# Optimization experiments

Hardware: AMD Instinct MI355X
Metric: run time of the kernel (lower is better)

## Reference

```python
import jax, jax.numpy as jnp
import numpy as np

# ---- problem dims (match init_kwargs / input_specs) ----
MC = 2048        # max_concepts
D = 128          # embed_dim
B = 64           # batch
L = 16           # program length
NOBJ = 128       # objects per scene
FDIM = 512       # feature_dim
NN = MC + NOBJ   # num_nodes
TEMP = 3.0       # cosine temperature
TH = 0.8         # true_th (cosine, train==val)
POS = 10.0
NEG = -10.0
YES_IDX = 0      # protocol['concepts','yes']
NO_IDX = 1       # protocol['concepts','no']
INIT_VAR = 0.001


def setup_inputs() -> dict:
    key = jax.random.key(0)
    ks = jax.random.split(key, 6)
    scene = jax.random.normal(ks[0], (B, NOBJ, FDIM), jnp.float32)
    # program[:, :, 0] = op code in [0,7), program[:, :, 1] = argument index
    program = jax.random.randint(ks[1], (B, L, 2), 0, 7, dtype=jnp.int32)
    concept_table = jax.random.normal(ks[2], (MC, D), jnp.float32) * INIT_VAR
    relation_table = jax.random.normal(ks[3], (MC, D * D), jnp.float32) * INIT_VAR
    W_feat = jax.random.normal(ks[4], (FDIM, D), jnp.float32) * INIT_VAR
    b_feat = jax.random.normal(ks[5], (D,), jnp.float32) * INIT_VAR
    return {"scene": scene, "program": program, "concept_table": concept_table,
            "relation_table": relation_table, "W_feat": W_feat, "b_feat": b_feat}


def _cos_sim(x, y, eps=1e-8):
    # torch F.cosine_similarity semantics: clamp each norm at eps
    xn = jnp.maximum(jnp.linalg.norm(x, axis=-1), eps)
    yn = jnp.maximum(jnp.linalg.norm(y, axis=-1), eps)
    return jnp.sum(x * y, axis=-1) / (xn * yn)


def reference(scene, program, concept_table, relation_table, W_feat, b_feat):
    # feature_mlp (dim_hidden == 0 -> single Linear)
    objects = scene @ W_feat + b_feat                              # [B, NOBJ, D]
    # per-step embedded arguments
    concept_args = concept_table[program[:, :, 1]]                 # [B, L, D]
    rel_args = relation_table[program[:, :, 1]].reshape(B, L, D, D)
    node_is_concept = jnp.arange(NN) < MC                          # [NN]
    # all_nodes = concat(all_concepts, objects) per sample
    all_nodes = jnp.concatenate(
        [jnp.broadcast_to(concept_table[None], (B, MC, D)), objects], axis=1)  # [B, NN, D]

    def run_sample(nodes_i, ops_i, args_i, cargs_i, rargs_i):
        att0 = jnp.ones((NN,), jnp.float32)

        def body(att, inp):
            op, arg, cvec, rmat = inp

            def f_null(a):
                return a

            def f_sel_obj(a):  # select 'object_only': zero concept slots
                return jnp.where(node_is_concept, 0.0, a)

            def f_sel_con(a):  # select 'concept_only': zero object slots
                return jnp.where(node_is_concept, a, 0.0)

            def f_verify(a):
                sim = _cos_sim(nodes_i, cvec[None, :])             # [NN]
                return jnp.minimum(a, jax.nn.sigmoid((sim - TH) * TEMP))

            def f_choose(a):
                a = jnp.where(node_is_concept, 0.0, a)
                return a.at[arg].set(1.0)

            def f_exist(a):
                s = a.max()
                yes = s * POS
                no = POS - yes
                a = jnp.full_like(a, NEG)
                return a.at[YES_IDX].set(yes).at[NO_IDX].set(no)

            def f_transfer(a):
                gather = a @ nodes_i                               # [D]
                trans = gather @ rmat                              # [D]
                sim = _cos_sim(nodes_i, trans[None, :])            # [NN]
                return jax.nn.sigmoid((sim - TH) * TEMP) * a.max()

            new = jax.lax.switch(
                op, [f_null, f_sel_obj, f_sel_con, f_verify, f_choose,
                     f_exist, f_transfer], att)
            return new, new

        _, hist = jax.lax.scan(body, att0, (ops_i, args_i, cargs_i, rargs_i))
        return hist                                                # [L, NN]

    hist = jax.vmap(run_sample)(all_nodes, program[:, :, 0], program[:, :, 1],
                                concept_args, rel_args)            # [B, L, NN]
    attn_final = hist[:, -1, :MC]                                  # [B, MC]
    out = jax.nn.log_softmax(attn_final, axis=1)
    return out, hist
```

## Files before the change

### kernel.cpp

```cpp
#include <hip/hip_runtime.h>
#include <math.h>

#define MC   2048
#define DD   128
#define BB   64
#define LL   16
#define NOBJ 128
#define FDIM 512
#define NN   (MC + NOBJ)
#define TEMPC 3.0f
#define THC   0.8f
#define POSC  10.0f
#define NEGC  (-10.0f)
#define EPSC  1e-8f
#define NARG  8
#define NINF  (-3.402823466e38f)
#define NSCALE 256.0f

#define QB   4
#define PART (NN / QB)
#define TS   512
#define NEP  32

typedef unsigned short ushort_t;
typedef float v2f __attribute__((ext_vector_type(2)));

#if defined(__has_builtin)
#if __has_builtin(__builtin_amdgcn_cvt_pk_f32_fp8)
#define HAS_HW_FP8 1
#endif
#endif

__device__ __forceinline__ float e4m3_dec1(unsigned int bv) {
    unsigned int s = (bv >> 7) & 1u, E = (bv >> 3) & 15u, M = bv & 7u;
    float v;
    if (E) v = __uint_as_float(((E + 120u) << 23) | (M << 20));
    else   v = (float)M * 0.001953125f;
    return s ? -v : v;
}
__device__ __forceinline__ v2f f8pair_sw(unsigned int w) {
    v2f r; r[0] = e4m3_dec1(w & 0xffu); r[1] = e4m3_dec1((w >> 8) & 0xffu); return r;
}
#ifdef HAS_HW_FP8
#define F8LO(u) __builtin_amdgcn_cvt_pk_f32_fp8((u), false)
#define F8HI(u) __builtin_amdgcn_cvt_pk_f32_fp8((u), true)
#else
#define F8LO(u) f8pair_sw((u) & 0xffffu)
#define F8HI(u) f8pair_sw((u) >> 16)
#endif

__device__ __forceinline__ unsigned int f32_to_e4m3(float x) {
    float a = fabsf(x);
    unsigned int s = (__float_as_uint(x) >> 31) << 7;
    if (a == 0.0f) return s;
    if (a >= 448.0f) return s | 0x7Eu;
    int e; float m = frexpf(a, &e);
    if (e >= -5) {
        int mant = (int)rintf(m * 16.0f);
        if (mant == 16) { mant = 8; e++; if (e - 1 > 8) return s | 0x7Eu; }
        return s | ((unsigned)(e - 1 + 7) << 3) | (unsigned)(mant - 8);
    } else {
        int q = (int)rintf(a * 512.0f);
        if (q >= 8) return s | 0x08u;
        return s | (unsigned)q;
    }
}

#define DEC16(u, g) do { \
    v2f _p0 = F8LO((u).x), _p1 = F8HI((u).x), _p2 = F8LO((u).y), _p3 = F8HI((u).y); \
    v2f _p4 = F8LO((u).z), _p5 = F8HI((u).z), _p6 = F8LO((u).w), _p7 = F8HI((u).w); \
    g[0]=_p0[0]; g[1]=_p0[1]; g[2]=_p1[0];  g[3]=_p1[1]; \
    g[4]=_p2[0]; g[5]=_p2[1]; g[6]=_p3[0];  g[7]=_p3[1]; \
    g[8]=_p4[0]; g[9]=_p4[1]; g[10]=_p5[0]; g[11]=_p5[1]; \
    g[12]=_p6[0]; g[13]=_p6[1]; g[14]=_p7[0]; g[15]=_p7[1]; \
} while (0)

__global__ __launch_bounds__(256) void gemm_objects(
        const float* __restrict__ scene, const float* __restrict__ W,
        const float* __restrict__ bias, float* __restrict__ obj) {
    __shared__ float sA[64][68];
    __shared__ float sB[64][68];
    const int b  = blockIdx.y;
    const int mt = (blockIdx.x >> 1) * 64;
    const int nt = (blockIdx.x & 1) * 64;
    const int tid = threadIdx.x;
    const int tx = tid & 15, ty = tid >> 4;
    float acc[4][4] = {{0.f,0.f,0.f,0.f},{0.f,0.f,0.f,0.f},{0.f,0.f,0.f,0.f},{0.f,0.f,0.f,0.f}};
    const float* sc = scene + (size_t)b * NOBJ * FDIM;
    for (int k0 = 0; k0 < FDIM; k0 += 64) {
        {
            const int o  = tid >> 2;
            const int ks = (tid & 3) * 16;
            const float4* src = (const float4*)(sc + (size_t)(mt + o) * FDIM + k0 + ks);
            #pragma unroll
            for (int j4 = 0; j4 < 4; j4++) {
                float4 v = src[j4];
                sA[ks + j4*4 + 0][o] = v.x;
                sA[ks + j4*4 + 1][o] = v.y;
                sA[ks + j4*4 + 2][o] = v.z;
                sA[ks + j4*4 + 3][o] = v.w;
            }
        }
        {
            const int kk = tid >> 2;
            const int dq = (tid & 3) * 16;
            const float4* src = (const float4*)(W + (size_t)(k0 + kk) * DD + nt + dq);
            float4* dst = (float4*)&sB[kk][dq];
            #pragma unroll
            for (int j4 = 0; j4 < 4; j4++) dst[j4] = src[j4];
        }
        __syncthreads();
        #pragma unroll 8
        for (int kk = 0; kk < 64; kk++) {
            float4 a4 = *(const float4*)&sA[kk][ty * 4];
            float4 b4 = *(const float4*)&sB[kk][tx * 4];
            float av[4] = {a4.x, a4.y, a4.z, a4.w};
            float bv[4] = {b4.x, b4.y, b4.z, b4.w};
            #pragma unroll
            for (int i = 0; i < 4; i++)
                #pragma unroll
                for (int j = 0; j < 4; j++)
                    acc[i][j] = fmaf(av[i], bv[j], acc[i][j]);
        }
        __syncthreads();
    }
    #pragma unroll
    for (int i = 0; i < 4; i++) {
        const int o = mt + ty * 4 + i;
        float4 r;
        r.x = acc[i][0] + bias[nt + tx*4 + 0];
        r.y = acc[i][1] + bias[nt + tx*4 + 1];
        r.z = acc[i][2] + bias[nt + tx*4 + 2];
        r.w = acc[i][3] + bias[nt + tx*4 + 3];
        *(float4*)(obj + ((size_t)b * NOBJ + o) * DD + nt + tx*4) = r;
    }
}

#define NBN ((MC + BB * NOBJ) / 4)

__global__ __launch_bounds__(256) void prep_fused(
        const float* __restrict__ ct, const float* __restrict__ obj,
        float* __restrict__ cnorm, float* __restrict__ onorm,
        unsigned char* __restrict__ ctf8, unsigned char* __restrict__ objf8,
        unsigned int* __restrict__ flags,
        float* __restrict__ sigc, float* __restrict__ sigo) {
    if (blockIdx.x < NBN) {
        if (blockIdx.x == 0) {
            for (int i = threadIdx.x; i < BB * NEP * QB; i += 256) flags[i] = 0u;
        }
        const int wid = threadIdx.x >> 6, lane = threadIdx.x & 63;
        const int r = blockIdx.x * 4 + wid;
        const float* row = (r < MC) ? (ct + (size_t)r * DD) : (obj + (size_t)(r - MC) * DD);
        unsigned char* brow = (r < MC) ? (ctf8 + (size_t)r * DD) : (objf8 + (size_t)(r - MC) * DD);
        float2 xy = *(const float2*)(row + lane * 2);
        float ss = xy.x * xy.x + xy.y * xy.y;
        #pragma unroll
        for (int off = 32; off; off >>= 1) ss += __shfl_xor(ss, off, 64);
        float nrm = fmaxf(sqrtf(ss), EPSC);
        float inv = NSCALE / nrm;
        unsigned int b0 = f32_to_e4m3(xy.x * inv);
        unsigned int b1 = f32_to_e4m3(xy.y * inv);
        *(ushort_t*)(brow + lane * 2) = (ushort_t)(b0 | (b1 << 8));
        if (lane == 0) {
            if (r < MC) cnorm[r] = nrm;
            else        onorm[r - MC] = nrm;
        }
        return;
    }
    __shared__ float cv[NARG][DD];
    __shared__ float cn[NARG];
    const int tid = threadIdx.x;
    for (int a = 0; a < NARG; a++)
        for (int i = tid; i < DD; i += 256) cv[a][i] = ct[(size_t)a * DD + i];
    __syncthreads();
    if (tid < NARG) {
        float ss = 0.f;
        for (int i = 0; i < DD; i++) ss = fmaf(cv[tid][i], cv[tid][i], ss);
        cn[tid] = fmaxf(sqrtf(ss), EPSC);
    }
    __syncthreads();
    const int sub = tid & 7, slot = tid >> 3;
    #pragma unroll
    for (int p = 0; p < 2; p++) {
        const int r = (blockIdx.x - NBN) * 64 + p * 32 + slot;
        const float* row = (r < MC) ? (ct + (size_t)r * DD) : (obj + (size_t)(r - MC) * DD);
        float4 r0 = *(const float4*)(row + sub * 16 + 0);
        float4 r1 = *(const float4*)(row + sub * 16 + 4);
        float4 r2 = *(const float4*)(row + sub * 16 + 8);
        float4 r3 = *(const float4*)(row + sub * 16 + 12);
        float ssr = 0.f;
        ssr = fmaf(r0.x, r0.x, ssr); ssr = fmaf(r0.y, r0.y, ssr);
        ssr = fmaf(r0.z, r0.z, ssr); ssr = fmaf(r0.w, r0.w, ssr);
        ssr = fmaf(r1.x, r1.x, ssr); ssr = fmaf(r1.y, r1.y, ssr);
        ssr = fmaf(r1.z, r1.z, ssr); ssr = fmaf(r1.w, r1.w, ssr);
        ssr = fmaf(r2.x, r2.x, ssr); ssr = fmaf(r2.y, r2.y, ssr);
        ssr = fmaf(r2.z, r2.z, ssr); ssr = fmaf(r2.w, r2.w, ssr);
        ssr = fmaf(r3.x, r3.x, ssr); ssr = fmaf(r3.y, r3.y, ssr);
        ssr = fmaf(r3.z, r3.z, ssr); ssr = fmaf(r3.w, r3.w, ssr);
        ssr += __shfl_xor(ssr, 1, 64);
        ssr += __shfl_xor(ssr, 2, 64);
        ssr += __shfl_xor(ssr, 4, 64);
        float rn = fmaxf(sqrtf(ssr), EPSC);
        for (int a = 0; a < NARG; a++) {
            const float* c = &cv[a][sub * 16];
            float dp = 0.f;
            dp = fmaf(r0.x, c[0], dp);  dp = fmaf(r0.y, c[1], dp);
            dp = fmaf(r0.z, c[2], dp);  dp = fmaf(r0.w, c[3], dp);
            dp = fmaf(r1.x, c[4], dp);  dp = fmaf(r1.y, c[5], dp);
            dp = fmaf(r1.z, c[6], dp);  dp = fmaf(r1.w, c[7], dp);
            dp = fmaf(r2.x, c[8], dp);  dp = fmaf(r2.y, c[9], dp);
            dp = fmaf(r2.z, c[10], dp); dp = fmaf(r2.w, c[11], dp);
            dp = fmaf(r3.x, c[12], dp); dp = fmaf(r3.y, c[13], dp);
            dp = fmaf(r3.z, c[14], dp); dp = fmaf(r3.w, c[15], dp);
            dp += __shfl_xor(dp, 1, 64);
            dp += __shfl_xor(dp, 2, 64);
            dp += __shfl_xor(dp, 4, 64);
            if (sub == 0) {
                float sim = dp / (rn * cn[a]);
                float g = 1.f / (1.f + __expf(-(sim - THC) * TEMPC));
                if (r < MC) sigc[(size_t)a * MC + r] = g;
                else {
                    int ro = r - MC, bb = ro >> 7, oo = ro & 127;
                    sigo[((size_t)bb * NARG + a) * NOBJ + oo] = g;
                }
            }
        }
    }
}


#define GATH_ROW(row_) do { \
    const int _r = (row_); \
    uint4 _u = *(const uint4*)&nd[_r * DD + ((sub ^ (_r & 7)) << 4)]; \
    const float _a = att[_r] * nrmL[_r]; \
    float _g[16]; DEC16(_u, _g); \
    _Pragma("unroll") \
    for (int _j = 0; _j < 16; _j++) ac[_j] = fmaf(_a, _g[_j], ac[_j]); \
} while (0)

#define SIM_ROW(row_, COMB) do { \
    const int _r = (row_); \
    uint4 _u = *(const uint4*)&nd[_r * DD + ((sub ^ (_r & 7)) << 4)]; \
    float _g[16]; DEC16(_u, _g); \
    float _dp = 0.f; \
    _Pragma("unroll") \
    for (int _j = 0; _j < 16; _j++) _dp = fmaf(_g[_j], vv[_j], _dp); \
    _dp += __shfl_xor(_dp, 1, 64); \
    _dp += __shfl_xor(_dp, 2, 64); \
    _dp += __shfl_xor(_dp, 4, 64); \
    if (sub == 0) { \
        const float _sim = _dp * invden; \
        const float sg = 1.f / (1.f + __expf(-(_sim - THC) * TEMPC)); \
        COMB; \
    } \
} while (0)

#define AST(p, v) __hip_atomic_store((p), (v), __ATOMIC_RELAXED, __HIP_MEMORY_SCOPE_AGENT)
#define ALD(p)    __hip_atomic_load((p), __ATOMIC_RELAXED, __HIP_MEMORY_SCOPE_AGENT)

#define QBARRIER() do { \
    __syncthreads(); \
    if (tid == 0) { \
        unsigned int* _fl = myflag + (int)epoch * QB; \
        AST(&_fl[q], 1u); \
        unsigned _s; \
        do { _s = ALD(&_fl[0]) + ALD(&_fl[1]) + ALD(&_fl[2]) + ALD(&_fl[3]); } while (_s < 4u); \
    } \
    __syncthreads(); \
} while (0)

__global__ __launch_bounds__(TS) void scan_exec(
        const float* __restrict__ ct, const float* __restrict__ rt,
        const int* __restrict__ program,
        const float* __restrict__ cnorm, const float* __restrict__ onorm,
        const float* __restrict__ sigc, const float* __restrict__ sigo,
        const unsigned char* __restrict__ ctf8, const unsigned char* __restrict__ objf8,
        float* __restrict__ gpart, unsigned int* __restrict__ flags,
        float* __restrict__ out, float* __restrict__ hist) {

    const int b    = blockIdx.x & (BB - 1);
    const int q    = blockIdx.x >> 6;
    const int base = q * PART;
    const int tid  = threadIdx.x;
    const int lane = tid & 63, wid = tid >> 6;
    const int rg   = tid >> 3, sub = tid & 7;

    __shared__ __align__(16) unsigned char nd[PART * DD];
    __shared__ __align__(16) float histL[LL * PART];
    __shared__ __align__(16) float att[PART];
    __shared__ __align__(16) float nrmL[PART];
    __shared__ __align__(16) float vec[DD];
    __shared__ __align__(16) float gvf[DD];
    __shared__ __align__(16) float part[8 * DD];
    __shared__ float wred[8];
    __shared__ float red2[8];
    __shared__ float s_sh;
    __shared__ float s_sh2;
    __shared__ int   sprog[2 * LL];

    const unsigned char* myobjf8 = objf8 + (size_t)b * NOBJ * DD;

    for (int idx = tid; idx < PART * 8; idx += TS) {
        const int row = idx >> 3, j = idx & 7;
        const int g   = base + row;
        const unsigned char* src = (g < MC) ? (ctf8 + (size_t)g * DD)
                                            : (myobjf8 + (size_t)(g - MC) * DD);
        uint4 v = *(const uint4*)(src + j * 16);
        *(uint4*)&nd[row * DD + ((j ^ (row & 7)) << 4)] = v;
    }
    for (int i = tid; i < PART; i += TS) {
        const int g = base + i;
        att[i]  = 1.0f;
        nrmL[i] = (g < MC) ? cnorm[g] : onorm[b * NOBJ + (g - MC)];
    }
    if (tid < 2 * LL) sprog[tid] = program[b * 2 * LL + tid];
    __syncthreads();

    unsigned int epoch = 0;
    float* gpb = gpart + (size_t)b * (2 * QB * 132);
    unsigned int* myflag = flags + b * (NEP * QB);

    for (int step = 0; step < LL; step++) {
        const int op  = sprog[2 * step];
        const int arg = sprog[2 * step + 1];
        float* hL = histL + step * PART;

        if (op == 0) {
            for (int i = tid; i < PART; i += TS) hL[i] = att[i];
        } else if (op == 1) {
            for (int i = tid; i < PART; i += TS) {
                const int g = base + i;
                const float nv = (g < MC) ? 0.0f : att[i];
                att[i] = nv; hL[i] = nv;
            }
        } else if (op == 2) {
            for (int i = tid; i < PART; i += TS) {
                const int g = base + i;
                const float nv = (g < MC) ? att[i] : 0.0f;
                att[i] = nv; hL[i] = nv;
            }
        } else if (op == 3 && arg < NARG) {
            const float* sc = sigc + (size_t)arg * MC;
            const float* so = sigo + ((size_t)b * NARG + arg) * NOBJ;
            for (int i = tid; i < PART; i += TS) {
                const int g = base + i;
                const float gg = (g < MC) ? sc[g] : so[g - MC];
                const float nv = fminf(att[i], gg);
                att[i] = nv; hL[i] = nv;
            }
        } else if (op == 3) {
            __syncthreads();
            if (tid < DD) vec[tid] = ct[(size_t)arg * DD + tid];
            __syncthreads();
            const float cn = fmaxf(cnorm[arg], EPSC);
            const float invden = 1.0f / (NSCALE * cn);
            float vv[16];
            {
                const float4 v0 = *(const float4*)&vec[sub * 16 + 0];
                const float4 v1 = *(const float4*)&vec[sub * 16 + 4];
                const float4 v2 = *(const float4*)&vec[sub * 16 + 8];
                const float4 v3 = *(const float4*)&vec[sub * 16 + 12];
                vv[0]=v0.x; vv[1]=v0.y; vv[2]=v0.z; vv[3]=v0.w;
                vv[4]=v1.x; vv[5]=v1.y; vv[6]=v1.z; vv[7]=v1.w;
                vv[8]=v2.x; vv[9]=v2.y; vv[10]=v2.z; vv[11]=v2.w;
                vv[12]=v3.x; vv[13]=v3.y; vv[14]=v3.z; vv[15]=v3.w;
            }
            #pragma unroll
            for (int p = 0; p < 8; p++)
                SIM_ROW(rg + p * 64, { const float nv = fminf(att[_r], sg); att[_r] = nv; hL[_r] = nv; });
            if (rg < PART - 512)
                SIM_ROW(rg + 512, { const float nv = fminf(att[_r], sg); att[_r] = nv; hL[_r] = nv; });
            __syncthreads();
        } else if (op == 4) {
            for (int i = tid; i < PART; i += TS) {
                const int g = base + i;
                const float nv = (g < MC) ? ((g == arg) ? 1.0f : 0.0f) : att[i];
                att[i] = nv; hL[i] = nv;
            }
        } else if (op == 5) {
            __syncthreads();
            float lm = NINF;
            for (int i = tid; i < PART; i += TS) lm = fmaxf(lm, att[i]);
            #pragma unroll
            for (int off = 32; off; off >>= 1) lm = fmaxf(lm, __shfl_xor(lm, off, 64));
            if (lane == 0) wred[wid] = lm;
            __syncthreads();
            epoch++;
            if (tid == 0) {
                float m = wred[0];
                #pragma unroll
                for (int w = 1; w < 8; w++) m = fmaxf(m, wred[w]);
                AST(&gpb[(size_t)((epoch & 1) * QB + q) * 132 + DD], m);
            }
            QBARRIER();
            if (tid == 0) {
                float* slotR = gpb + (size_t)((epoch & 1) * QB) * 132;
                float m = NINF;
                #pragma unroll
                for (int k = 0; k < QB; k++)
                    m = fmaxf(m, ALD(&slotR[k * 132 + DD]));
                s_sh = m;
            }
            __syncthreads();
            const float s = s_sh;
            const float yes = s * POSC, no = POSC - yes;
            for (int i = tid; i < PART; i += TS) {
                const int g = base + i;
                const float nv = (g == 0) ? yes : ((g == 1) ? no : NEGC);
                att[i] = nv; hL[i] = nv;
            }
        } else if (op == 6) {
            __syncthreads();
            const float* rm = rt + (size_t)arg * (DD * DD);
            const int half = lane >> 5, dq = (lane & 31) * 4;
            float4 rmr[8];
            #pragma unroll
            for (int j = 0; j < 8; j++) {
                const int d = wid * 16 + half * 8 + j;
                rmr[j] = *(const float4*)(rm + (size_t)d * DD + dq);
            }
            float lm = NINF;
            for (int i = tid; i < PART; i += TS) lm = fmaxf(lm, att[i]);
            #pragma unroll
            for (int off = 32; off; off >>= 1) lm = fmaxf(lm, __shfl_xor(lm, off, 64));
            if (lane == 0) wred[wid] = lm;
            float ac[16];
            #pragma unroll
            for (int j = 0; j < 16; j++) ac[j] = 0.f;
            #pragma unroll
            for (int p = 0; p < 8; p++) GATH_ROW(rg + p * 64);
            if (rg < PART - 512) GATH_ROW(rg + 512);
            #pragma unroll
            for (int j = 0; j < 16; j++) {
                ac[j] += __shfl_xor(ac[j], 8, 64);
                ac[j] += __shfl_xor(ac[j], 16, 64);
                ac[j] += __shfl_xor(ac[j], 32, 64);
            }
            if (lane < 8) {
                float* dst = &part[wid * DD + lane * 16];
                #pragma unroll
                for (int k = 0; k < 4; k++)
                    *(float4*)(dst + k * 4) = make_float4(ac[k*4], ac[k*4+1], ac[k*4+2], ac[k*4+3]);
            }
            __syncthreads();
            epoch++;
            {
                float* slotW = gpb + (size_t)((epoch & 1) * QB + q) * 132;
                if (tid < DD) {
                    float gsum = 0.f;
                    #pragma unroll
                    for (int w = 0; w < 8; w++) gsum += part[w * DD + tid];
                    AST(&slotW[tid], gsum);
                }
                if (tid == DD) {
                    float m = wred[0];
                    #pragma unroll
                    for (int w = 1; w < 8; w++) m = fmaxf(m, wred[w]);
                    AST(&slotW[DD], m);
                }
            }
            QBARRIER();
            {
                float* slotR = gpb + (size_t)((epoch & 1) * QB) * 132;
                if (tid < DD) {
                    float gsum = 0.f;
                    #pragma unroll
                    for (int k = 0; k < QB; k++)
                        gsum += ALD(&slotR[k * 132 + tid]);
                    gvf[tid] = gsum;
                }
                if (tid == DD) {
                    float m = NINF;
                    #pragma unroll
                    for (int k = 0; k < QB; k++)
                        m = fmaxf(m, ALD(&slotR[k * 132 + DD]));
                    s_sh = m;
                }
            }
            __syncthreads();
            float qx = 0.f, qy = 0.f, qz = 0.f, qw = 0.f;
            #pragma unroll
            for (int j = 0; j < 8; j++) {
                const int d = wid * 16 + half * 8 + j;
                const float g = gvf[d];
                qx = fmaf(g, rmr[j].x, qx); qy = fmaf(g, rmr[j].y, qy);
                qz = fmaf(g, rmr[j].z, qz); qw = fmaf(g, rmr[j].w, qw);
            }
            qx += __shfl_xor(qx, 32, 64); qy += __shfl_xor(qy, 32, 64);
            qz += __shfl_xor(qz, 32, 64); qw += __shfl_xor(qw, 32, 64);
            if (lane < 32) *(float4*)&part[wid * DD + dq] = make_float4(qx, qy, qz, qw);
            __syncthreads();
            if (tid < DD) {
                float t = 0.f;
                #pragma unroll
                for (int w = 0; w < 8; w++) t += part[w * DD + tid];
                vec[tid] = t;
                float ss = t * t;
                #pragma unroll
                for (int off = 32; off; off >>= 1) ss += __shfl_xor(ss, off, 64);
                if (lane == 0) red2[wid] = ss;
            }
            __syncthreads();
            const float tn = fmaxf(sqrtf(red2[0] + red2[1]), EPSC * NSCALE);
            const float invden = 1.0f / (NSCALE * tn);
            const float s = s_sh;
            float vv[16];
            {
                const float4 v0 = *(const float4*)&vec[sub * 16 + 0];
                const float4 v1 = *(const float4*)&vec[sub * 16 + 4];
                const float4 v2 = *(const float4*)&vec[sub * 16 + 8];
                const float4 v3 = *(const float4*)&vec[sub * 16 + 12];
                vv[0]=v0.x; vv[1]=v0.y; vv[2]=v0.z; vv[3]=v0.w;
                vv[4]=v1.x; vv[5]=v1.y; vv[6]=v1.z; vv[7]=v1.w;
                vv[8]=v2.x; vv[9]=v2.y; vv[10]=v2.z; vv[11]=v2.w;
                vv[12]=v3.x; vv[13]=v3.y; vv[14]=v3.z; vv[15]=v3.w;
            }
            #pragma unroll
            for (int p = 0; p < 8; p++)
                SIM_ROW(rg + p * 64, { const float nv = sg * s; att[_r] = nv; hL[_r] = nv; });
            if (rg < PART - 512)
                SIM_ROW(rg + 512, { const float nv = sg * s; att[_r] = nv; hL[_r] = nv; });
            __syncthreads();
        }
    }

    __syncthreads();
    {
        const int nf4 = PART / 4;
        for (int idx = tid; idx < LL * nf4; idx += TS) {
            const int step = idx / nf4;
            const int i4   = idx - step * nf4;
            *(float4*)(hist + ((size_t)b * LL + step) * NN + base + i4 * 4) =
                *(const float4*)&histL[step * PART + i4 * 4];
        }
    }

    const int crows = (base + PART <= MC) ? PART : (MC - base);
    {
        float lm = NINF;
        for (int i = tid; i < crows; i += TS) lm = fmaxf(lm, att[i]);
        #pragma unroll
        for (int off = 32; off; off >>= 1) lm = fmaxf(lm, __shfl_xor(lm, off, 64));
        if (lane == 0) wred[wid] = lm;
    }
    __syncthreads();
    float mloc = wred[0];
    #pragma unroll
    for (int w = 1; w < 8; w++) mloc = fmaxf(mloc, wred[w]);
    {
        float lse = 0.f;
        for (int i = tid; i < crows; i += TS) lse += expf(att[i] - mloc);
        #pragma unroll
        for (int off = 32; off; off >>= 1) lse += __shfl_xor(lse, off, 64);
        if (lane == 0) red2[wid] = lse;
    }
    __syncthreads();
    epoch++;
    if (tid == 0) {
        float sloc = 0.f;
        #pragma unroll
        for (int w = 0; w < 8; w++) sloc += red2[w];
        float* slotW = gpb + (size_t)((epoch & 1) * QB + q) * 132;
        AST(&slotW[DD], mloc);
        AST(&slotW[DD + 1], sloc);
    }
    QBARRIER();
    if (tid == 0) {
        float* slotR = gpb + (size_t)((epoch & 1) * QB) * 132;
        float mg = NINF;
        float mq[QB], sq[QB];
        #pragma unroll
        for (int k = 0; k < QB; k++) {
            mq[k] = ALD(&slotR[k * 132 + DD]);
            sq[k] = ALD(&slotR[k * 132 + DD + 1]);
            mg = fmaxf(mg, mq[k]);
        }
        float se = 0.f;
        #pragma unroll
        for (int k = 0; k < QB; k++) se += sq[k] * expf(mq[k] - mg);
        s_sh  = mg;
        s_sh2 = logf(se);
    }
    __syncthreads();
    const float mglob = s_sh, ls = s_sh2;
    for (int i = tid; i < crows; i += TS)
        out[(size_t)b * MC + base + i] = att[i] - mglob - ls;
}

extern "C" void kernel_launch(void* const* d_in, const int* in_sizes, int n_in,
                              void* d_out, int out_size, void* d_ws, size_t ws_size,
                              hipStream_t stream) {
    const float* scene = (const float*)d_in[0];
    const int*   prog  = (const int*)d_in[1];
    const float* ct    = (const float*)d_in[2];
    const float* rt    = (const float*)d_in[3];
    const float* W     = (const float*)d_in[4];
    const float* bias  = (const float*)d_in[5];

    float* out  = (float*)d_out;
    float* hist = out + (size_t)BB * MC;

    float* obj   = (float*)d_ws;
    float* cnorm = obj + (size_t)BB * NOBJ * DD;
    float* onorm = cnorm + MC;
    float* sigc  = onorm + (size_t)BB * NOBJ;
    float* sigo  = sigc + (size_t)NARG * MC;
    float* gpart = sigo + (size_t)BB * NARG * NOBJ;
    unsigned int* flagbuf = (unsigned int*)(gpart + (size_t)BB * 2 * QB * 132);
    unsigned char* ctf8  = (unsigned char*)(flagbuf + BB * NEP * QB);
    unsigned char* objf8 = ctf8 + (size_t)MC * DD;

    gemm_objects<<<dim3(4, BB), 256, 0, stream>>>(scene, W, bias, obj);
    prep_fused<<<dim3(NBN + (MC + BB * NOBJ) / 64), 256, 0, stream>>>(
        ct, obj, cnorm, onorm, ctf8, objf8, flagbuf, sigc, sigo);
    scan_exec<<<dim3(BB * QB), TS, 0, stream>>>(ct, rt, prog, cnorm, onorm, sigc, sigo,
                                                ctf8, objf8, gpart, flagbuf, out, hist);
}
```

Before: 262.6 us.

## Fuse object GEMM with norm/FP8/sigmoid prep and stream history directly to global

Merges the object-feature GEMM and the prep kernel into one launch. The GEMM epilogue now computes row norms, the FP8 quantisation and the per-argument sigmoid scores straight from registers, so the fp32 object matrix is never written to or reread from the workspace. The scan kernel also drops its large shared-memory history buffer and writes each step's attention straight to global memory, which frees LDS and removes the final copy loop. In exchange the history stores become scalar and spread across steps, and the GEMM tiles are smaller (32 rows per block), which may lower per-block efficiency.

```diff
diff --git a/kernel.cpp b/kernel.cpp
--- a/kernel.cpp
+++ b/kernel.cpp
@@ -75,83 +75,135 @@
     g[12]=_p6[0]; g[13]=_p6[1]; g[14]=_p7[0]; g[15]=_p7[1]; \
 } while (0)
 
-__global__ __launch_bounds__(256) void gemm_objects(
+#define GEMB 256
+#define CONB 512
+#define SIGB 64
+
+__global__ __launch_bounds__(256) void prep_all(
         const float* __restrict__ scene, const float* __restrict__ W,
-        const float* __restrict__ bias, float* __restrict__ obj) {
-    __shared__ float sA[64][68];
-    __shared__ float sB[64][68];
-    const int b  = blockIdx.y;
-    const int mt = (blockIdx.x >> 1) * 64;
-    const int nt = (blockIdx.x & 1) * 64;
-    const int tid = threadIdx.x;
-    const int tx = tid & 15, ty = tid >> 4;
-    float acc[4][4] = {{0.f,0.f,0.f,0.f},{0.f,0.f,0.f,0.f},{0.f,0.f,0.f,0.f},{0.f,0.f,0.f,0.f}};
-    const float* sc = scene + (size_t)b * NOBJ * FDIM;
-    for (int k0 = 0; k0 < FDIM; k0 += 64) {
-        {
-            const int o  = tid >> 2;
-            const int ks = (tid & 3) * 16;
-            const float4* src = (const float4*)(sc + (size_t)(mt + o) * FDIM + k0 + ks);
-            #pragma unroll
-            for (int j4 = 0; j4 < 4; j4++) {
-                float4 v = src[j4];
-                sA[ks + j4*4 + 0][o] = v.x;
-                sA[ks + j4*4 + 1][o] = v.y;
-                sA[ks + j4*4 + 2][o] = v.z;
-                sA[ks + j4*4 + 3][o] = v.w;
-            }
-        }
-        {
-            const int kk = tid >> 2;
-            const int dq = (tid & 3) * 16;
-            const float4* src = (const float4*)(W + (size_t)(k0 + kk) * DD + nt + dq);
-            float4* dst = (float4*)&sB[kk][dq];
-            #pragma unroll
-            for (int j4 = 0; j4 < 4; j4++) dst[j4] = src[j4];
-        }
-        __syncthreads();
-        #pragma unroll 8
-        for (int kk = 0; kk < 64; kk++) {
-            float4 a4 = *(const float4*)&sA[kk][ty * 4];
-            float4 b4 = *(const float4*)&sB[kk][tx * 4];
-            float av[4] = {a4.x, a4.y, a4.z, a4.w};
-            float bv[4] = {b4.x, b4.y, b4.z, b4.w};
-            #pragma unroll
-            for (int i = 0; i < 4; i++)
-                #pragma unroll
-                for (int j = 0; j < 4; j++)
-                    acc[i][j] = fmaf(av[i], bv[j], acc[i][j]);
-        }
-        __syncthreads();
-    }
-    #pragma unroll
-    for (int i = 0; i < 4; i++) {
-        const int o = mt + ty * 4 + i;
-        float4 r;
-        r.x = acc[i][0] + bias[nt + tx*4 + 0];
-        r.y = acc[i][1] + bias[nt + tx*4 + 1];
-        r.z = acc[i][2] + bias[nt + tx*4 + 2];
-        r.w = acc[i][3] + bias[nt + tx*4 + 3];
-        *(float4*)(obj + ((size_t)b * NOBJ + o) * DD + nt + tx*4) = r;
-    }
-}
-
-#define NBN ((MC + BB * NOBJ) / 4)
-
-__global__ __launch_bounds__(256) void prep_fused(
-        const float* __restrict__ ct, const float* __restrict__ obj,
+        const float* __restrict__ bias, const float* __restrict__ ct,
         float* __restrict__ cnorm, float* __restrict__ onorm,
         unsigned char* __restrict__ ctf8, unsigned char* __restrict__ objf8,
-        unsigned int* __restrict__ flags,
-        float* __restrict__ sigc, float* __restrict__ sigo) {
-    if (blockIdx.x < NBN) {
-        if (blockIdx.x == 0) {
-            for (int i = threadIdx.x; i < BB * NEP * QB; i += 256) flags[i] = 0u;
-        }
-        const int wid = threadIdx.x >> 6, lane = threadIdx.x & 63;
-        const int r = blockIdx.x * 4 + wid;
-        const float* row = (r < MC) ? (ct + (size_t)r * DD) : (obj + (size_t)(r - MC) * DD);
-        unsigned char* brow = (r < MC) ? (ctf8 + (size_t)r * DD) : (objf8 + (size_t)(r - MC) * DD);
+        float* __restrict__ sigc, float* __restrict__ sigo,
+        unsigned int* __restrict__ flags) {
+    const int blk = blockIdx.x;
+    const int tid = threadIdx.x;
+
+    if (blk < GEMB) {
+        __shared__ float sA[64][36];
+        __shared__ float sB[64][132];
+        __shared__ float cv[NARG][DD];
+        __shared__ float cnn[NARG];
+        const int b = blk >> 2, q3 = blk & 3;
+        const int row0 = q3 * 32;
+        if (blk == 0) {
+            for (int i = tid; i < BB * NEP * QB; i += 256) flags[i] = 0u;
+        }
+        for (int i = tid; i < NARG * DD; i += 256) cv[i >> 7][i & 127] = ct[i];
+        __syncthreads();
+        if (tid < NARG) {
+            float ss = 0.f;
+            for (int i = 0; i < DD; i++) ss = fmaf(cv[tid][i], cv[tid][i], ss);
+            cnn[tid] = fmaxf(sqrtf(ss), EPSC);
+        }
+        const int tx = tid & 31, ty = tid >> 5;
+        float acc[4][4] = {{0.f,0.f,0.f,0.f},{0.f,0.f,0.f,0.f},{0.f,0.f,0.f,0.f},{0.f,0.f,0.f,0.f}};
+        const float* sc = scene + ((size_t)b * NOBJ + row0) * FDIM;
+        for (int k0 = 0; k0 < FDIM; k0 += 64) {
+            {
+                const int r = tid >> 3, kq = (tid & 7) * 8;
+                const float* src = sc + (size_t)r * FDIM + k0 + kq;
+                float4 v0 = *(const float4*)(src);
+                float4 v1 = *(const float4*)(src + 4);
+                sA[kq+0][r]=v0.x; sA[kq+1][r]=v0.y; sA[kq+2][r]=v0.z; sA[kq+3][r]=v0.w;
+                sA[kq+4][r]=v1.x; sA[kq+5][r]=v1.y; sA[kq+6][r]=v1.z; sA[kq+7][r]=v1.w;
+            }
+            {
+                const int kk = tid >> 2, colq = (tid & 3) * 32;
+                const float* src = W + (size_t)(k0 + kk) * DD + colq;
+                float4* dst = (float4*)&sB[kk][colq];
+                #pragma unroll
+                for (int j = 0; j < 8; j++) dst[j] = *(const float4*)(src + j * 4);
+            }
+            __syncthreads();
+            #pragma unroll 8
+            for (int kk = 0; kk < 64; kk++) {
+                float4 a4 = *(const float4*)&sA[kk][ty * 4];
+                float4 b4 = *(const float4*)&sB[kk][tx * 4];
+                float av[4] = {a4.x, a4.y, a4.z, a4.w};
+                float bv[4] = {b4.x, b4.y, b4.z, b4.w};
+                #pragma unroll
+                for (int i = 0; i < 4; i++)
+                    #pragma unroll
+                    for (int j = 0; j < 4; j++)
+                        acc[i][j] = fmaf(av[i], bv[j], acc[i][j]);
+            }
+            __syncthreads();
+        }
+        {
+            float4 bb4 = *(const float4*)(bias + tx * 4);
+            float bv[4] = {bb4.x, bb4.y, bb4.z, bb4.w};
+            #pragma unroll
+            for (int i = 0; i < 4; i++)
+                #pragma unroll
+                for (int j = 0; j < 4; j++) acc[i][j] += bv[j];
+        }
+        float nrm4[4], inv4[4];
+        #pragma unroll
+        for (int i = 0; i < 4; i++) {
+            float ss = 0.f;
+            #pragma unroll
+            for (int j = 0; j < 4; j++) ss = fmaf(acc[i][j], acc[i][j], ss);
+            ss += __shfl_xor(ss, 1, 32);  ss += __shfl_xor(ss, 2, 32);
+            ss += __shfl_xor(ss, 4, 32);  ss += __shfl_xor(ss, 8, 32);
+            ss += __shfl_xor(ss, 16, 32);
+            nrm4[i] = fmaxf(sqrtf(ss), EPSC);
+            inv4[i] = NSCALE / nrm4[i];
+        }
+        const int grow = b * NOBJ + row0 + ty * 4;
+        #pragma unroll
+        for (int i = 0; i < 4; i++) {
+            unsigned int w = f32_to_e4m3(acc[i][0] * inv4[i])
+                           | (f32_to_e4m3(acc[i][1] * inv4[i]) << 8)
+                           | (f32_to_e4m3(acc[i][2] * inv4[i]) << 16)
+                           | (f32_to_e4m3(acc[i][3] * inv4[i]) << 24);
+            *(unsigned int*)(objf8 + (size_t)(grow + i) * DD + tx * 4) = w;
+        }
+        if (tx == 0) {
+            #pragma unroll
+            for (int i = 0; i < 4; i++) onorm[grow + i] = nrm4[i];
+        }
+        #pragma unroll
+        for (int a = 0; a < NARG; a++) {
+            float dp[4];
+            #pragma unroll
+            for (int i = 0; i < 4; i++) {
+                float d = 0.f;
+                d = fmaf(acc[i][0], cv[a][tx*4+0], d);
+                d = fmaf(acc[i][1], cv[a][tx*4+1], d);
+                d = fmaf(acc[i][2], cv[a][tx*4+2], d);
+                d = fmaf(acc[i][3], cv[a][tx*4+3], d);
+                d += __shfl_xor(d, 1, 32);  d += __shfl_xor(d, 2, 32);
+                d += __shfl_xor(d, 4, 32);  d += __shfl_xor(d, 8, 32);
+                d += __shfl_xor(d, 16, 32);
+                dp[i] = d;
+            }
+            if (tx == 0) {
+                #pragma unroll
+                for (int i = 0; i < 4; i++) {
+                    float sim = dp[i] / (nrm4[i] * cnn[a]);
+                    float g = 1.f / (1.f + __expf(-(sim - THC) * TEMPC));
+                    sigo[((size_t)b * NARG + a) * NOBJ + row0 + ty * 4 + i] = g;
+                }
+            }
+        }
+        return;
+    }
+
+    if (blk < GEMB + CONB) {
+        const int wid = tid >> 6, lane = tid & 63;
+        const int r = (blk - GEMB) * 4 + wid;
+        const float* row = ct + (size_t)r * DD;
         float2 xy = *(const float2*)(row + lane * 2);
         float ss = xy.x * xy.x + xy.y * xy.y;
         #pragma unroll
@@ -160,70 +212,60 @@
         float inv = NSCALE / nrm;
         unsigned int b0 = f32_to_e4m3(xy.x * inv);
         unsigned int b1 = f32_to_e4m3(xy.y * inv);
-        *(ushort_t*)(brow + lane * 2) = (ushort_t)(b0 | (b1 << 8));
-        if (lane == 0) {
-            if (r < MC) cnorm[r] = nrm;
-            else        onorm[r - MC] = nrm;
-        }
+        *(ushort_t*)(ctf8 + (size_t)r * DD + lane * 2) = (ushort_t)(b0 | (b1 << 8));
+        if (lane == 0) cnorm[r] = nrm;
         return;
     }
-    __shared__ float cv[NARG][DD];
-    __shared__ float cn[NARG];
-    const int tid = threadIdx.x;
+
+    __shared__ float cv2[NARG][DD];
+    __shared__ float cn2[NARG];
     for (int a = 0; a < NARG; a++)
-        for (int i = tid; i < DD; i += 256) cv[a][i] = ct[(size_t)a * DD + i];
+        for (int i = tid; i < DD; i += 256) cv2[a][i] = ct[(size_t)a * DD + i];
     __syncthreads();
     if (tid < NARG) {
         float ss = 0.f;
-        for (int i = 0; i < DD; i++) ss = fmaf(cv[tid][i], cv[tid][i], ss);
-        cn[tid] = fmaxf(sqrtf(ss), EPSC);
+        for (int i = 0; i < DD; i++) ss = fmaf(cv2[tid][i], cv2[tid][i], ss);
+        cn2[tid] = fmaxf(sqrtf(ss), EPSC);
     }
     __syncthreads();
     const int sub = tid & 7, slot = tid >> 3;
-    #pragma unroll
-    for (int p = 0; p < 2; p++) {
-        const int r = (blockIdx.x - NBN) * 64 + p * 32 + slot;
-        const float* row = (r < MC) ? (ct + (size_t)r * DD) : (obj + (size_t)(r - MC) * DD);
-        float4 r0 = *(const float4*)(row + sub * 16 + 0);
-        float4 r1 = *(const float4*)(row + sub * 16 + 4);
-        float4 r2 = *(const float4*)(row + sub * 16 + 8);
-        float4 r3 = *(const float4*)(row + sub * 16 + 12);
-        float ssr = 0.f;
-        ssr = fmaf(r0.x, r0.x, ssr); ssr = fmaf(r0.y, r0.y, ssr);
-        ssr = fmaf(r0.z, r0.z, ssr); ssr = fmaf(r0.w, r0.w, ssr);
-        ssr = fmaf(r1.x, r1.x, ssr); ssr = fmaf(r1.y, r1.y, ssr);
-        ssr = fmaf(r1.z, r1.z, ssr); ssr = fmaf(r1.w, r1.w, ssr);
-        ssr = fmaf(r2.x, r2.x, ssr); ssr = fmaf(r2.y, r2.y, ssr);
-        ssr = fmaf(r2.z, r2.z, ssr); ssr = fmaf(r2.w, r2.w, ssr);
-        ssr = fmaf(r3.x, r3.x, ssr); ssr = fmaf(r3.y, r3.y, ssr);
-        ssr = fmaf(r3.z, r3.z, ssr); ssr = fmaf(r3.w, r3.w, ssr);
-        ssr += __shfl_xor(ssr, 1, 64);
-        ssr += __shfl_xor(ssr, 2, 64);
-        ssr += __shfl_xor(ssr, 4, 64);
-        float rn = fmaxf(sqrtf(ssr), EPSC);
-        for (int a = 0; a < NARG; a++) {
-            const float* c = &cv[a][sub * 16];
-            float dp = 0.f;
-            dp = fmaf(r0.x, c[0], dp);  dp = fmaf(r0.y, c[1], dp);
-            dp = fmaf(r0.z, c[2], dp);  dp = fmaf(r0.w, c[3], dp);
-            dp = fmaf(r1.x, c[4], dp);  dp = fmaf(r1.y, c[5], dp);
-            dp = fmaf(r1.z, c[6], dp);  dp = fmaf(r1.w, c[7], dp);
-            dp = fmaf(r2.x, c[8], dp);  dp = fmaf(r2.y, c[9], dp);
-            dp = fmaf(r2.z, c[10], dp); dp = fmaf(r2.w, c[11], dp);
-            dp = fmaf(r3.x, c[12], dp); dp = fmaf(r3.y, c[13], dp);
-            dp = fmaf(r3.z, c[14], dp); dp = fmaf(r3.w, c[15], dp);
-            dp += __shfl_xor(dp, 1, 64);
-            dp += __shfl_xor(dp, 2, 64);
-            dp += __shfl_xor(dp, 4, 64);
-            if (sub == 0) {
-                float sim = dp / (rn * cn[a]);
-                float g = 1.f / (1.f + __expf(-(sim - THC) * TEMPC));
-                if (r < MC) sigc[(size_t)a * MC + r] = g;
-                else {
-                    int ro = r - MC, bb = ro >> 7, oo = ro & 127;
-                    sigo[((size_t)bb * NARG + a) * NOBJ + oo] = g;
-                }
-            }
+    const int r = (blk - GEMB - CONB) * 32 + slot;
+    const float* row = ct + (size_t)r * DD;
+    float4 r0 = *(const float4*)(row + sub * 16 + 0);
+    float4 r1 = *(const float4*)(row + sub * 16 + 4);
+    float4 r2 = *(const float4*)(row + sub * 16 + 8);
+    float4 r3 = *(const float4*)(row + sub * 16 + 12);
+    float ssr = 0.f;
+    ssr = fmaf(r0.x, r0.x, ssr); ssr = fmaf(r0.y, r0.y, ssr);
+    ssr = fmaf(r0.z, r0.z, ssr); ssr = fmaf(r0.w, r0.w, ssr);
+    ssr = fmaf(r1.x, r1.x, ssr); ssr = fmaf(r1.y, r1.y, ssr);
+    ssr = fmaf(r1.z, r1.z, ssr); ssr = fmaf(r1.w, r1.w, ssr);
+    ssr = fmaf(r2.x, r2.x, ssr); ssr = fmaf(r2.y, r2.y, ssr);
+    ssr = fmaf(r2.z, r2.z, ssr); ssr = fmaf(r2.w, r2.w, ssr);
+    ssr = fmaf(r3.x, r3.x, ssr); ssr = fmaf(r3.y, r3.y, ssr);
+    ssr = fmaf(r3.z, r3.z, ssr); ssr = fmaf(r3.w, r3.w, ssr);
+    ssr += __shfl_xor(ssr, 1, 64);
+    ssr += __shfl_xor(ssr, 2, 64);
+    ssr += __shfl_xor(ssr, 4, 64);
+    float rn = fmaxf(sqrtf(ssr), EPSC);
+    for (int a = 0; a < NARG; a++) {
+        const float* c = &cv2[a][sub * 16];
+        float dp = 0.f;
+        dp = fmaf(r0.x, c[0], dp);  dp = fmaf(r0.y, c[1], dp);
+        dp = fmaf(r0.z, c[2], dp);  dp = fmaf(r0.w, c[3], dp);
+        dp = fmaf(r1.x, c[4], dp);  dp = fmaf(r1.y, c[5], dp);
+        dp = fmaf(r1.z, c[6], dp);  dp = fmaf(r1.w, c[7], dp);
+        dp = fmaf(r2.x, c[8], dp);  dp = fmaf(r2.y, c[9], dp);
+        dp = fmaf(r2.z, c[10], dp); dp = fmaf(r2.w, c[11], dp);
+        dp = fmaf(r3.x, c[12], dp); dp = fmaf(r3.y, c[13], dp);
+        dp = fmaf(r3.z, c[14], dp); dp = fmaf(r3.w, c[15], dp);
+        dp += __shfl_xor(dp, 1, 64);
+        dp += __shfl_xor(dp, 2, 64);
+        dp += __shfl_xor(dp, 4, 64);
+        if (sub == 0) {
+            float sim = dp / (rn * cn2[a]);
+            float g = 1.f / (1.f + __expf(-(sim - THC) * TEMPC));
+            sigc[(size_t)a * MC + r] = g;
         }
     }
 }
@@ -286,7 +328,6 @@
     const int rg   = tid >> 3, sub = tid & 7;
 
     __shared__ __align__(16) unsigned char nd[PART * DD];
-    __shared__ __align__(16) float histL[LL * PART];
     __shared__ __align__(16) float att[PART];
     __shared__ __align__(16) float nrmL[PART];
     __shared__ __align__(16) float vec[DD];
@@ -323,21 +364,21 @@
     for (int step = 0; step < LL; step++) {
         const int op  = sprog[2 * step];
         const int arg = sprog[2 * step + 1];
-        float* hL = histL + step * PART;
+        float* hrow = hist + ((size_t)b * LL + step) * NN;
 
         if (op == 0) {
-            for (int i = tid; i < PART; i += TS) hL[i] = att[i];
+            for (int i = tid; i < PART; i += TS) hrow[base + i] = att[i];
         } else if (op == 1) {
             for (int i = tid; i < PART; i += TS) {
                 const int g = base + i;
                 const float nv = (g < MC) ? 0.0f : att[i];
-                att[i] = nv; hL[i] = nv;
+                att[i] = nv; hrow[g] = nv;
             }
         } else if (op == 2) {
             for (int i = tid; i < PART; i += TS) {
                 const int g = base + i;
                 const float nv = (g < MC) ? att[i] : 0.0f;
-                att[i] = nv; hL[i] = nv;
+                att[i] = nv; hrow[g] = nv;
             }
         } else if (op == 3 && arg < NARG) {
             const float* sc = sigc + (size_t)arg * MC;
@@ -346,7 +387,7 @@
                 const int g = base + i;
                 const float gg = (g < MC) ? sc[g] : so[g - MC];
                 const float nv = fminf(att[i], gg);
-                att[i] = nv; hL[i] = nv;
+                att[i] = nv; hrow[g] = nv;
             }
         } else if (op == 3) {
             __syncthreads();
@@ -367,15 +408,15 @@
             }
             #pragma unroll
             for (int p = 0; p < 8; p++)
-                SIM_ROW(rg + p * 64, { const float nv = fminf(att[_r], sg); att[_r] = nv; hL[_r] = nv; });
+                SIM_ROW(rg + p * 64, { const float nv = fminf(att[_r], sg); att[_r] = nv; hrow[base + _r] = nv; });
             if (rg < PART - 512)
-                SIM_ROW(rg + 512, { const float nv = fminf(att[_r], sg); att[_r] = nv; hL[_r] = nv; });
+                SIM_ROW(rg + 512, { const float nv = fminf(att[_r], sg); att[_r] = nv; hrow[base + _r] = nv; });
             __syncthreads();
         } else if (op == 4) {
             for (int i = tid; i < PART; i += TS) {
                 const int g = base + i;
                 const float nv = (g < MC) ? ((g == arg) ? 1.0f : 0.0f) : att[i];
-                att[i] = nv; hL[i] = nv;
+                att[i] = nv; hrow[g] = nv;
             }
         } else if (op == 5) {
             __syncthreads();
@@ -407,7 +448,7 @@
             for (int i = tid; i < PART; i += TS) {
                 const int g = base + i;
                 const float nv = (g == 0) ? yes : ((g == 1) ? no : NEGC);
-                att[i] = nv; hL[i] = nv;
+                att[i] = nv; hrow[g] = nv;
             }
         } else if (op == 6) {
             __syncthreads();
@@ -517,22 +558,13 @@
             }
             #pragma unroll
             for (int p = 0; p < 8; p++)
-                SIM_ROW(rg + p * 64, { const float nv = sg * s; att[_r] = nv; hL[_r] = nv; });
+                SIM_ROW(rg + p * 64, { const float nv = sg * s; att[_r] = nv; hrow[base + _r] = nv; });
             if (rg < PART - 512)
-                SIM_ROW(rg + 512, { const float nv = sg * s; att[_r] = nv; hL[_r] = nv; });
-            __syncthreads();
-        }
-    }
-
-    __syncthreads();
-    {
-        const int nf4 = PART / 4;
-        for (int idx = tid; idx < LL * nf4; idx += TS) {
-            const int step = idx / nf4;
-            const int i4   = idx - step * nf4;
-            *(float4*)(hist + ((size_t)b * LL + step) * NN + base + i4 * 4) =
-                *(const float4*)&histL[step * PART + i4 * 4];
-        }
+                SIM_ROW(rg + 512, { const float nv = sg * s; att[_r] = nv; hrow[base + _r] = nv; });
+            __syncthreads();
+        }
+
+        __syncthreads();
     }
 
     const int crows = (base + PART <= MC) ? PART : (MC - base);
@@ -600,8 +632,7 @@
     float* out  = (float*)d_out;
     float* hist = out + (size_t)BB * MC;
 
-    float* obj   = (float*)d_ws;
-    float* cnorm = obj + (size_t)BB * NOBJ * DD;
+    float* cnorm = (float*)d_ws;
     float* onorm = cnorm + MC;
     float* sigc  = onorm + (size_t)BB * NOBJ;
     float* sigo  = sigc + (size_t)NARG * MC;
@@ -610,9 +641,8 @@
     unsigned char* ctf8  = (unsigned char*)(flagbuf + BB * NEP * QB);
     unsigned char* objf8 = ctf8 + (size_t)MC * DD;
 
-    gemm_objects<<<dim3(4, BB), 256, 0, stream>>>(scene, W, bias, obj);
-    prep_fused<<<dim3(NBN + (MC + BB * NOBJ) / 64), 256, 0, stream>>>(
-        ct, obj, cnorm, onorm, ctf8, objf8, flagbuf, sigc, sigo);
+    prep_all<<<dim3(GEMB + CONB + SIGB), 256, 0, stream>>>(
+        scene, W, bias, ct, cnorm, onorm, ctf8, objf8, sigc, sigo, flagbuf);
     scan_exec<<<dim3(BB * QB), TS, 0, stream>>>(ct, rt, prog, cnorm, onorm, sigc, sigo,
                                                 ctf8, objf8, gpart, flagbuf, out, hist);
 }
```

Result: no change. 261.5 us (-0.4%).
